# Optimization experiments

Hardware: AMD Instinct MI355X
Metric: run time of the kernel (lower is better)

## Reference

```python
import jax, jax.numpy as jnp
import numpy as np

N_ATOMS = 100000
N_EDGES = 400000
ATOM_DIM = 32
BOND_DIM = 16


def setup_inputs() -> dict:
    key = jax.random.key(0)
    k1, k2, k3, k4 = jax.random.split(key, 4)
    atom_features = jax.random.normal(k1, (N_ATOMS, ATOM_DIM), dtype=jnp.float32)
    bond_features = jax.random.normal(k2, (N_EDGES, BOND_DIM), dtype=jnp.float32)
    pair_indices = jax.random.randint(k3, (N_EDGES, 2), 0, N_ATOMS, dtype=jnp.int64)
    # glorot-uniform-like scale for the kernel
    limit = np.sqrt(6.0 / (BOND_DIM + ATOM_DIM * ATOM_DIM)).astype(np.float32)
    kernel = jax.random.uniform(k4, (BOND_DIM, ATOM_DIM * ATOM_DIM), dtype=jnp.float32,
                                minval=-limit, maxval=limit)
    bias = jnp.zeros((ATOM_DIM * ATOM_DIM,), dtype=jnp.float32)
    return {"atom_features": atom_features, "bond_features": bond_features,
            "pair_indices": pair_indices, "kernel": kernel, "bias": bias}


def reference(atom_features, bond_features, pair_indices, kernel, bias):
    n_atoms, d = atom_features.shape  # d = atom_dim
    e = bond_features.shape[0]
    # per-edge transform matrices: [E, d, d]
    edge_mats = (bond_features @ kernel + bias).reshape(e, d, d)
    # gather neighbor atom features via pair_indices[:, 1]
    neighbors = atom_features[pair_indices[:, 1]]  # [E, d]
    # per-edge matvec
    transformed = jnp.einsum('eij,ej->ei', edge_mats, neighbors)  # [E, d]
    # scatter-reduce onto source atoms
    return jax.ops.segment_sum(transformed, pair_indices[:, 0], num_segments=n_atoms)
```

## Files before the change

### kernel.cpp

```cpp
#include <hip/hip_runtime.h>
#include <hip/hip_fp16.h>


typedef _Float16 half8 __attribute__((ext_vector_type(8)));
typedef _Float16 half4t __attribute__((ext_vector_type(4)));
typedef float float4v __attribute__((ext_vector_type(4)));

constexpr int NA = 100000;
constexpr int E  = 400000;
constexpr int TILES = E / 32;
constexpr int NBLK  = 768;
constexpr int HALFW = NBLK * 4 / 2;

constexpr size_t OFF_ATOMH = 0;
constexpr size_t OFF_BONDH = (size_t)NA * 32 * 2;
constexpr size_t OFF_ACC   = OFF_BONDH + (size_t)E*16*2;

constexpr int NZ4 = NA * 32 / 4;
constexpr int NA4 = NA * 32 / 4;
constexpr int NB4 = E * 16 / 4;
constexpr int PREP_TOT = NZ4 + NA4 + NB4;

__global__ void k_prep(const float* __restrict__ atom,
                       const float* __restrict__ bond,
                       half4t* __restrict__ accz,
                       half4t* __restrict__ atomh4,
                       half4t* __restrict__ bondh4) {
  int i = blockIdx.x * 256 + threadIdx.x;
  if (i < NZ4) {
    half4t z = { (_Float16)0.f, (_Float16)0.f, (_Float16)0.f, (_Float16)0.f };
    accz[i] = z;
  } else if (i < NZ4 + NA4) {
    int k = i - NZ4;
    float4 v = ((const float4*)atom)[k];
    half4t hh = { (_Float16)v.x, (_Float16)v.y, (_Float16)v.z, (_Float16)v.w };
    atomh4[k] = hh;
  } else if (i < PREP_TOT) {
    int k = i - NZ4 - NA4;
    float4 v = ((const float4*)bond)[k];
    half4t hh = { (_Float16)v.x, (_Float16)v.y, (_Float16)v.z, (_Float16)v.w };
    bondh4[k] = hh;
  }
}

static __device__ inline half8 splat8(_Float16 v) {
  half8 r = {v, v, v, v, v, v, v, v};
  return r;
}

__global__ __launch_bounds__(256, 3)
void edge_fused(const _Float16* __restrict__ atomh,
                const _Float16* __restrict__ bondh,
                const int* __restrict__ pairs,
                const float* __restrict__ Kmat,
                const float* __restrict__ bias,
                _Float16* __restrict__ accum)
{
  const int tid  = threadIdx.x;
  const int lane = tid & 63;
  const int wid  = blockIdx.x * 4 + (tid >> 6);
  const int h    = wid & 1;
  const int q    = lane >> 4;
  const int el   = lane & 15;
  const int n    = el + h * 16;
  const int j0   = q * 8;

  half8 Wr[17];
  #pragma unroll
  for (int s = 0; s < 17; ++s) {
    const float* src = (s < 16) ? (Kmat + s * 1024 + n * 32 + j0)
                                : (bias + n * 32 + j0);
    half8 w;
    #pragma unroll
    for (int j = 0; j < 8; ++j) w[j] = (_Float16)src[j];
    Wr[s] = w;
  }

  const int start  = wid >> 1;
  const int stride = HALFW;
  const int2* pairs2 = (const int2*)pairs;

  auto ldpv = [&](int t) -> int2 {
    const int tc = t < TILES ? t : TILES - 1;
    int2 v = make_int2(0, 0);
    if (lane < 32) v = pairs2[tc * 32 + lane];
    return v;
  };

  int2 pv0 = ldpv(start);
  int2 pv1 = ldpv(start + stride);

  half8 nbA_c, nbB_c, bA0_c, bA1_c, bB0_c, bB1_c;
  {
    const int aA = __shfl(pv0.y, el);
    const int aB = __shfl(pv0.y, el + 16);
    nbA_c = *(const half8*)(atomh + (size_t)aA * 32 + j0);
    nbB_c = *(const half8*)(atomh + (size_t)aB * 32 + j0);
    const _Float16* brA = bondh + (size_t)(start * 32 + el) * 16;
    const _Float16* brB = bondh + (size_t)(start * 32 + el + 16) * 16;
    bA0_c = *(const half8*)(brA);  bA1_c = *(const half8*)(brA + 8);
    bB0_c = *(const half8*)(brB);  bB1_c = *(const half8*)(brB + 8);
  }

  for (int t = start; t < TILES; t += stride) {
    const int tn = t + stride;

    half8 nbA_n, nbB_n, bA0_n, bA1_n, bB0_n, bB1_n;
    {
      const int aA = __shfl(pv1.y, el);
      const int aB = __shfl(pv1.y, el + 16);
      nbA_n = *(const half8*)(atomh + (size_t)aA * 32 + j0);
      nbB_n = *(const half8*)(atomh + (size_t)aB * 32 + j0);
      const int tc = tn < TILES ? tn : TILES - 1;
      const _Float16* brA = bondh + (size_t)(tc * 32 + el) * 16;
      const _Float16* brB = bondh + (size_t)(tc * 32 + el + 16) * 16;
      bA0_n = *(const half8*)(brA);  bA1_n = *(const half8*)(brA + 8);
      bB0_n = *(const half8*)(brB);  bB1_n = *(const half8*)(brB + 8);
    }
    const int2 pv2 = ldpv(tn + stride);

    float4v acc0 = {0.f, 0.f, 0.f, 0.f};
    float4v acc1 = {0.f, 0.f, 0.f, 0.f};
    #pragma unroll
    for (int s = 0; s < 16; ++s) {
      const _Float16 sA = (s < 8) ? bA0_c[s] : bA1_c[s - 8];
      const _Float16 sB = (s < 8) ? bB0_c[s] : bB1_c[s - 8];
      const half8 aAf = nbA_c * splat8(sA);
      const half8 aBf = nbB_c * splat8(sB);
      acc0 = __builtin_amdgcn_mfma_f32_16x16x32_f16(aAf, Wr[s], acc0, 0, 0, 0);
      acc1 = __builtin_amdgcn_mfma_f32_16x16x32_f16(aBf, Wr[s], acc1, 0, 0, 0);
    }
    acc0 = __builtin_amdgcn_mfma_f32_16x16x32_f16(nbA_c, Wr[16], acc0, 0, 0, 0);
    acc1 = __builtin_amdgcn_mfma_f32_16x16x32_f16(nbB_c, Wr[16], acc1, 0, 0, 0);

    #pragma unroll
    for (int r = 0; r < 4; ++r) {
      {
        const int   s0 = __shfl(pv0.x, q * 4 + r);
        const float v  = acc0[r];
        const float pvx = __shfl_xor(v, 1);
        if (!(el & 1)) {
          union { _Float16 f[2]; __half2 h; } u;
          u.f[0] = (_Float16)v; u.f[1] = (_Float16)pvx;
          unsafeAtomicAdd(
              reinterpret_cast<__half2*>(accum + (size_t)s0 * 32 + n), u.h);
        }
      }
      {
        const int   s1 = __shfl(pv0.x, q * 4 + r + 16);
        const float v  = acc1[r];
        const float pvx = __shfl_xor(v, 1);
        if (!(el & 1)) {
          union { _Float16 f[2]; __half2 h; } u;
          u.f[0] = (_Float16)v; u.f[1] = (_Float16)pvx;
          unsafeAtomicAdd(
              reinterpret_cast<__half2*>(accum + (size_t)s1 * 32 + n), u.h);
        }
      }
    }

    pv0 = pv1; pv1 = pv2;
    nbA_c = nbA_n; nbB_c = nbB_n;
    bA0_c = bA0_n; bA1_c = bA1_n; bB0_c = bB0_n; bB1_c = bB1_n;
  }
}

__global__ void k_fin(const half4t* __restrict__ acc4,
                      float4* __restrict__ out4) {
  int i = blockIdx.x * 256 + threadIdx.x;
  if (i >= NZ4) return;
  half4t v = acc4[i];
  out4[i] = make_float4((float)v[0], (float)v[1], (float)v[2], (float)v[3]);
}

extern "C" void kernel_launch(void* const* d_in, const int* in_sizes, int n_in,
                              void* d_out, int out_size, void* d_ws, size_t ws_size,
                              hipStream_t stream) {
  const float* atom  = (const float*)d_in[0];
  const float* bondf = (const float*)d_in[1];
  const int*   pairs = (const int*)d_in[2];
  const float* Kmat  = (const float*)d_in[3];
  const float* bias  = (const float*)d_in[4];
  float* out = (float*)d_out;

  char* ws = (char*)d_ws;
  _Float16* atomh = (_Float16*)(ws + OFF_ATOMH);
  _Float16* bondh = (_Float16*)(ws + OFF_BONDH);
  _Float16* accum = (_Float16*)(ws + OFF_ACC);

  k_prep<<<(PREP_TOT + 255) / 256, 256, 0, stream>>>(
      atom, bondf, (half4t*)accum, (half4t*)atomh, (half4t*)bondh);
  edge_fused<<<NBLK, 256, 0, stream>>>(atomh, bondh, pairs, Kmat, bias, accum);
  k_fin<<<(NZ4 + 255) / 256, 256, 0, stream>>>((const half4t*)accum,
                                               (float4*)out);
}
```

Measured before the change: 146.7 us.

## Process 16-edge groups per wave computing all 32 outputs, weights split regs/LDS

Each wave now handles 16 edges and computes all 32 output columns, instead of two waves sharing 32 edges and each covering 16 output columns. The first half of the weights stays in registers and the second half is staged in LDS with a padded stride, read once per MFMA step. Each wave now forms the scaled neighbor operand once and reuses it for both column halves, which halves the duplicated elementwise scaling work and the neighbor gathers. All lanes now take part in the packed half2 atomics. The trade-off is added LDS traffic and a block-wide barrier at startup.

```diff
diff --git a/kernel.cpp b/kernel.cpp
--- a/kernel.cpp
+++ b/kernel.cpp
@@ -8,9 +8,9 @@
 
 constexpr int NA = 100000;
 constexpr int E  = 400000;
-constexpr int TILES = E / 32;
+constexpr int GRP   = E / 16;
 constexpr int NBLK  = 768;
-constexpr int HALFW = NBLK * 4 / 2;
+constexpr int NWAVE = NBLK * 4;
 
 constexpr size_t OFF_ATOMH = 0;
 constexpr size_t OFF_BONDH = (size_t)NA * 32 * 2;
@@ -20,6 +20,8 @@
 constexpr int NA4 = NA * 32 / 4;
 constexpr int NB4 = E * 16 / 4;
 constexpr int PREP_TOT = NZ4 + NA4 + NB4;
+
+constexpr int WSTRIDE = 80;
 
 __global__ void k_prep(const float* __restrict__ atom,
                        const float* __restrict__ bond,
@@ -56,112 +58,112 @@
                 const float* __restrict__ bias,
                 _Float16* __restrict__ accum)
 {
+  __shared__ __attribute__((aligned(16))) char wl[17 * 16 * WSTRIDE];
+
   const int tid  = threadIdx.x;
   const int lane = tid & 63;
   const int wid  = blockIdx.x * 4 + (tid >> 6);
-  const int h    = wid & 1;
   const int q    = lane >> 4;
   const int el   = lane & 15;
-  const int n    = el + h * 16;
   const int j0   = q * 8;
+
+  for (int i4 = tid; i4 < 17 * 16 * 32 / 4; i4 += 256) {
+    const int i   = i4 * 4;
+    const int s   = i >> 9;
+    const int r   = i & 511;
+    const int n16 = r >> 5;
+    const int j   = r & 31;
+    const float* src = (s < 16) ? (Kmat + s * 1024 + (n16 + 16) * 32 + j)
+                                : (bias + (n16 + 16) * 32 + j);
+    float4 v = *(const float4*)src;
+    half4t hh = { (_Float16)v.x, (_Float16)v.y, (_Float16)v.z, (_Float16)v.w };
+    *(half4t*)(wl + (s * 16 + n16) * WSTRIDE + j * 2) = hh;
+  }
 
   half8 Wr[17];
   #pragma unroll
   for (int s = 0; s < 17; ++s) {
-    const float* src = (s < 16) ? (Kmat + s * 1024 + n * 32 + j0)
-                                : (bias + n * 32 + j0);
+    const float* src = (s < 16) ? (Kmat + s * 1024 + el * 32 + j0)
+                                : (bias + el * 32 + j0);
     half8 w;
     #pragma unroll
     for (int j = 0; j < 8; ++j) w[j] = (_Float16)src[j];
     Wr[s] = w;
   }
 
-  const int start  = wid >> 1;
-  const int stride = HALFW;
+  __syncthreads();
+
   const int2* pairs2 = (const int2*)pairs;
+  const char* wb = wl + el * WSTRIDE + q * 16;
 
-  auto ldpv = [&](int t) -> int2 {
-    const int tc = t < TILES ? t : TILES - 1;
+  auto ldpv = [&](int g) -> int2 {
+    const int gc = g < GRP ? g : GRP - 1;
     int2 v = make_int2(0, 0);
-    if (lane < 32) v = pairs2[tc * 32 + lane];
+    if (lane < 16) v = pairs2[gc * 16 + lane];
     return v;
   };
 
-  int2 pv0 = ldpv(start);
-  int2 pv1 = ldpv(start + stride);
+  int2 pv0 = ldpv(wid);
+  int2 pv1 = ldpv(wid + NWAVE);
 
-  half8 nbA_c, nbB_c, bA0_c, bA1_c, bB0_c, bB1_c;
+  half8 nb_c, b0_c, b1_c;
   {
-    const int aA = __shfl(pv0.y, el);
-    const int aB = __shfl(pv0.y, el + 16);
-    nbA_c = *(const half8*)(atomh + (size_t)aA * 32 + j0);
-    nbB_c = *(const half8*)(atomh + (size_t)aB * 32 + j0);
-    const _Float16* brA = bondh + (size_t)(start * 32 + el) * 16;
-    const _Float16* brB = bondh + (size_t)(start * 32 + el + 16) * 16;
-    bA0_c = *(const half8*)(brA);  bA1_c = *(const half8*)(brA + 8);
-    bB0_c = *(const half8*)(brB);  bB1_c = *(const half8*)(brB + 8);
+    const int a = __shfl(pv0.y, el);
+    nb_c = *(const half8*)(atomh + (size_t)a * 32 + j0);
+    const _Float16* br = bondh + (size_t)(wid * 16 + el) * 16;
+    b0_c = *(const half8*)(br);  b1_c = *(const half8*)(br + 8);
   }
 
-  for (int t = start; t < TILES; t += stride) {
-    const int tn = t + stride;
+  for (int g = wid; g < GRP; g += NWAVE) {
+    const int gn = g + NWAVE;
 
-    half8 nbA_n, nbB_n, bA0_n, bA1_n, bB0_n, bB1_n;
+    half8 nb_n, b0_n, b1_n;
     {
-      const int aA = __shfl(pv1.y, el);
-      const int aB = __shfl(pv1.y, el + 16);
-      nbA_n = *(const half8*)(atomh + (size_t)aA * 32 + j0);
-      nbB_n = *(const half8*)(atomh + (size_t)aB * 32 + j0);
-      const int tc = tn < TILES ? tn : TILES - 1;
-      const _Float16* brA = bondh + (size_t)(tc * 32 + el) * 16;
-      const _Float16* brB = bondh + (size_t)(tc * 32 + el + 16) * 16;
-      bA0_n = *(const half8*)(brA);  bA1_n = *(const half8*)(brA + 8);
-      bB0_n = *(const half8*)(brB);  bB1_n = *(const half8*)(brB + 8);
+      const int a = __shfl(pv1.y, el);
+      nb_n = *(const half8*)(atomh + (size_t)a * 32 + j0);
+      const int gc = gn < GRP ? gn : GRP - 1;
+      const _Float16* br = bondh + (size_t)(gc * 16 + el) * 16;
+      b0_n = *(const half8*)(br);  b1_n = *(const half8*)(br + 8);
     }
-    const int2 pv2 = ldpv(tn + stride);
+    const int2 pv2 = ldpv(gn + NWAVE);
 
-    float4v acc0 = {0.f, 0.f, 0.f, 0.f};
-    float4v acc1 = {0.f, 0.f, 0.f, 0.f};
+    int zz;
+    asm volatile("s_mov_b32 %0, 0" : "=s"(zz));
+    const char* wbz = wb + zz;
+
+    float4v a0 = {0.f, 0.f, 0.f, 0.f};
+    float4v a1 = {0.f, 0.f, 0.f, 0.f};
     #pragma unroll
     for (int s = 0; s < 16; ++s) {
-      const _Float16 sA = (s < 8) ? bA0_c[s] : bA1_c[s - 8];
-      const _Float16 sB = (s < 8) ? bB0_c[s] : bB1_c[s - 8];
-      const half8 aAf = nbA_c * splat8(sA);
-      const half8 aBf = nbB_c * splat8(sB);
-      acc0 = __builtin_amdgcn_mfma_f32_16x16x32_f16(aAf, Wr[s], acc0, 0, 0, 0);
-      acc1 = __builtin_amdgcn_mfma_f32_16x16x32_f16(aBf, Wr[s], acc1, 0, 0, 0);
+      const _Float16 sc = (s < 8) ? b0_c[s] : b1_c[s - 8];
+      const half8 af = nb_c * splat8(sc);
+      const half8 w1 = *(const half8*)(wbz + s * 16 * WSTRIDE);
+      a0 = __builtin_amdgcn_mfma_f32_16x16x32_f16(af, Wr[s], a0, 0, 0, 0);
+      a1 = __builtin_amdgcn_mfma_f32_16x16x32_f16(af, w1,    a1, 0, 0, 0);
     }
-    acc0 = __builtin_amdgcn_mfma_f32_16x16x32_f16(nbA_c, Wr[16], acc0, 0, 0, 0);
-    acc1 = __builtin_amdgcn_mfma_f32_16x16x32_f16(nbB_c, Wr[16], acc1, 0, 0, 0);
+    {
+      const half8 w1 = *(const half8*)(wbz + 16 * 16 * WSTRIDE);
+      a0 = __builtin_amdgcn_mfma_f32_16x16x32_f16(nb_c, Wr[16], a0, 0, 0, 0);
+      a1 = __builtin_amdgcn_mfma_f32_16x16x32_f16(nb_c, w1,     a1, 0, 0, 0);
+    }
 
+    const bool ev = !(el & 1);
     #pragma unroll
     for (int r = 0; r < 4; ++r) {
-      {
-        const int   s0 = __shfl(pv0.x, q * 4 + r);
-        const float v  = acc0[r];
-        const float pvx = __shfl_xor(v, 1);
-        if (!(el & 1)) {
-          union { _Float16 f[2]; __half2 h; } u;
-          u.f[0] = (_Float16)v; u.f[1] = (_Float16)pvx;
-          unsafeAtomicAdd(
-              reinterpret_cast<__half2*>(accum + (size_t)s0 * 32 + n), u.h);
-        }
-      }
-      {
-        const int   s1 = __shfl(pv0.x, q * 4 + r + 16);
-        const float v  = acc1[r];
-        const float pvx = __shfl_xor(v, 1);
-        if (!(el & 1)) {
-          union { _Float16 f[2]; __half2 h; } u;
-          u.f[0] = (_Float16)v; u.f[1] = (_Float16)pvx;
-          unsafeAtomicAdd(
-              reinterpret_cast<__half2*>(accum + (size_t)s1 * 32 + n), u.h);
-        }
-      }
+      const int   d  = __shfl(pv0.x, q * 4 + r);
+      const float v0 = a0[r], v1 = a1[r];
+      const float p0 = __shfl_xor(v0, 1);
+      const float p1 = __shfl_xor(v1, 1);
+      union { _Float16 f[2]; __half2 h; } u;
+      u.f[0] = ev ? (_Float16)v0 : (_Float16)p1;
+      u.f[1] = ev ? (_Float16)p0 : (_Float16)v1;
+      const int col = ev ? el : (15 + el);
+      unsafeAtomicAdd(reinterpret_cast<__half2*>(
+                          accum + (size_t)d * 32 + col), u.h);
     }
 
     pv0 = pv1; pv1 = pv2;
-    nbA_c = nbA_n; nbB_c = nbB_n;
-    bA0_c = bA0_n; bA1_c = bA1_n; bB0_c = bB0_n; bB1_c = bB1_n;
+    nb_c = nb_n; b0_c = b0_n; b1_c = b1_n;
   }
 }
 
```

Result: faster. 128.2 us (-12.6%).
